# Kernel optimization log

Measured on AMD Instinct MI355X. Metric: run time of the kernel, lower is better.

Reference implementation:

```python
import jax, jax.numpy as jnp
import numpy as np

N, W, T = 8, 64, 8192      # batch, emb_width, time
K_BINS = 2048

def setup_inputs() -> dict:
    key = jax.random.key(0)
    kx, kk = jax.random.split(key)
    x = jax.random.normal(kx, (N, W, T), dtype=jnp.float32)
    k = jax.random.normal(kk, (K_BINS, W), dtype=jnp.float32)
    return {"x": x, "k": k}

def reference(x, k):
    n, w, t = x.shape
    # preprocess: (N, W, T) -> (N*T, W)
    xf = jnp.transpose(x, (0, 2, 1)).reshape(-1, w)
    prenorm = jnp.linalg.norm(xf - jnp.mean(xf)) / np.sqrt(float(xf.size))
    # quantise: squared-euclidean distances via matmul expansion
    # dist[i, j] = ||xf_i||^2 - 2 xf_i . k_j + ||k_j||^2   -> (N*T, K_BINS)
    dist = (jnp.sum(xf * xf, axis=-1, keepdims=True)
            - 2.0 * (xf @ k.T)
            + jnp.sum(k * k, axis=-1)[None, :])
    x_l = jnp.argmin(dist, axis=-1)            # (N*T,)
    fit = jnp.mean(jnp.min(dist, axis=-1))
    # dequantise: embedding gather
    x_d = k[x_l]                               # (N*T, W)
    commit_loss = jnp.sum((jax.lax.stop_gradient(x_d) - xf) ** 2) / float(xf.size)
    # straight-through estimator
    x_d = xf + jax.lax.stop_gradient(x_d - xf)
    # postprocess
    x_l = x_l.reshape(n, t)
    x_d = jnp.transpose(x_d.reshape(n, t, w), (0, 2, 1))  # (N, W, T)
    return x_l, x_d, commit_loss, fit, prenorm
```

## Files before the change

kernel.cpp:

```cpp
#include <hip/hip_runtime.h>
#include <hip/hip_bf16.h>
#include <math.h>

#define N_BATCH 8
#define WDIM 64
#define TDIM 8192
#define KBINS 2048
#define NROWS (N_BATCH * TDIM)
#define XSIZE (N_BATCH * WDIM * TDIM)
#define XL_OFF 0
#define XD_OFF NROWS
#define SCAL_OFF (NROWS + XSIZE)

#define MT 64
#define XST 72
#define TAU 0.05f
#define MAXFLAG 8192
#define NBLK (NROWS / MT)

#define WS_K2_OFF   0
#define WS_CNT_OFF  8192
#define WS_FLAG_OFF 8256
#define WS_SLOT_OFF 41024
#define WS_PART_OFF 106560
#define WS_KF_OFF   122944

typedef __attribute__((ext_vector_type(8))) short bf16x8;
typedef __attribute__((ext_vector_type(4))) float f32x4;
typedef unsigned long long u64;

static __device__ __forceinline__ short f2bf(float v) {
  __hip_bfloat16 b = __float2bfloat16(v);
  return *reinterpret_cast<short*>(&b);
}
static __device__ __forceinline__ float bf2f(short s) {
  unsigned int u = ((unsigned int)(unsigned short)s) << 16;
  return __uint_as_float(u);
}

#define GLOAD_LDS(gsrc, ldst)                                            \
  __builtin_amdgcn_global_load_lds(                                      \
      (const __attribute__((address_space(1))) unsigned int*)(gsrc),     \
      (__attribute__((address_space(3))) unsigned int*)(ldst), 16, 0, 0)

#define WAIT_VM4 0x0F74
#define WAIT_VM0 0x0F70

__global__ void prep_kernel(const float* __restrict__ kg, float* __restrict__ k2,
                            char* __restrict__ kfrag,
                            int* __restrict__ cnt, u64* __restrict__ slots) {
  __shared__ float skc[16 * 65];
  const int tid  = threadIdx.x;
  const int tile = blockIdx.x;
  const int c0   = tile * 16;
  if (tile == 0 && tid == 0) *cnt = 0;
  if (tid < 64) slots[tile * 64 + tid] = ~0ULL;
  {
    const float4* g4 = (const float4*)(kg + (size_t)c0 * WDIM);
    int code = tid >> 4, w = (tid & 15) * 4;
    *(float4*)&skc[code * 65 + w] = g4[tid];
  }
  __syncthreads();
  if (tid < 16) {
    const float* kr = &skc[tid * 65];
    float r[8];
#pragma unroll
    for (int l = 0; l < 8; ++l) r[l] = __fmul_rn(kr[l], kr[l]);
    for (int i = 8; i < WDIM; i += 8) {
#pragma unroll
      for (int l = 0; l < 8; ++l)
        r[l] = __fadd_rn(r[l], __fmul_rn(kr[i + l], kr[i + l]));
    }
    k2[c0 + tid] = __fadd_rn(__fadd_rn(__fadd_rn(r[0], r[1]), __fadd_rn(r[2], r[3])),
                             __fadd_rn(__fadd_rn(r[4], r[5]), __fadd_rn(r[6], r[7])));
  }
  {
    const int sub  = tid >> 6;
    const int lane = tid & 63;
    const int lcol = lane & 15;
    const int quad = lane >> 4;
    const float* src = &skc[lcol * 65 + (sub & 1) * 32 + quad * 8];
    const bool lo = (sub >= 2);
    short tmp[8];
#pragma unroll
    for (int i = 0; i < 8; ++i) {
      float v = src[i];
      short h = f2bf(v);
      tmp[i] = lo ? f2bf(v - bf2f(h)) : h;
    }
    char* dst = kfrag + (size_t)tile * 4096 + sub * 1024 + lane * 16;
    *(bf16x8*)dst = *(const bf16x8*)tmp;
  }
}

__launch_bounds__(128, 2)
__global__ void vq_mfma(const float* __restrict__ x,
                        const float* __restrict__ kg,
                        const float* __restrict__ k2g,
                        const char* __restrict__ kfrag,
                        float* __restrict__ out,
                        float* __restrict__ part,
                        int* __restrict__ flag_cnt,
                        int* __restrict__ flags) {
  __shared__ __align__(16) char smem[33408];
  char*  kbuf  = smem;
  float* k2f   = (float*)(smem + 24576);
  int*   sIdx      = (int*)  (smem + 32768);
  float* sPair     = (float*)(smem + 33024);
  int*   sFlagCnt  = (int*)  (smem + 33088);
  int*   sFlagBase = (int*)  (smem + 33092);
  int*   sFlagList = (int*)  (smem + 33096);
  short* sxh = (short*)smem;
  short* sxl = (short*)(smem + 9216);
  float* kd  = (float*)smem;

  const int tid  = threadIdx.x;
  const int blk  = blockIdx.x;
  const int row0 = blk * MT;
  const int n    = row0 >> 13;
  const int t0   = row0 & (TDIM - 1);

  if (tid == 0) *sFlagCnt = 0;

  const int r  = tid & 63;
  const int wh = tid >> 6;
  float x2p = 0.f, sxp = 0.f;
  const float* xb = x + (size_t)n * WDIM * TDIM + t0 + r;
#pragma unroll 8
  for (int i = 0; i < 32; ++i) {
    int w = 2 * i + wh;
    float v = xb[(size_t)w * TDIM];
    x2p = fmaf(v, v, x2p);
    sxp += v;
    short h = f2bf(v);
    sxh[r * XST + w] = h;
    sxl[r * XST + w] = f2bf(v - bf2f(h));
  }
  {
    const float4* k24 = (const float4*)k2g;
#pragma unroll
    for (int i = 0; i < 4; ++i) {
      int j = tid + i * 128;
      *(float4*)&k2f[j * 4] = k24[j];
    }
  }
  __syncthreads();

  const int wave = tid >> 6;
  const int lane = tid & 63;
  const int lcol = lane & 15;
  const int quad = lane >> 4;
  const int rA0 = wave * 32 + lcol;
  const int rA1 = wave * 32 + 16 + lcol;
  bf16x8 a0h0 = *(const bf16x8*)&sxh[rA0 * XST + 0  + quad * 8];
  bf16x8 a0h1 = *(const bf16x8*)&sxh[rA0 * XST + 32 + quad * 8];
  bf16x8 a0l0 = *(const bf16x8*)&sxl[rA0 * XST + 0  + quad * 8];
  bf16x8 a0l1 = *(const bf16x8*)&sxl[rA0 * XST + 32 + quad * 8];
  bf16x8 a1h0 = *(const bf16x8*)&sxh[rA1 * XST + 0  + quad * 8];
  bf16x8 a1h1 = *(const bf16x8*)&sxh[rA1 * XST + 32 + quad * 8];
  bf16x8 a1l0 = *(const bf16x8*)&sxl[rA1 * XST + 0  + quad * 8];
  bf16x8 a1l1 = *(const bf16x8*)&sxl[rA1 * XST + 32 + quad * 8];
  __syncthreads();

  float bd[8], b2[8];
  int   bi[8];
#pragma unroll
  for (int i = 0; i < 8; ++i) { bd[i] = 3.0e38f; b2[i] = 3.0e38f; bi[i] = 0; }

  char* mybuf = kbuf + wave * 12288;
  const char* kfg = kfrag;

#define VQ_ISSUE(C, B)                                                       \
  if ((C) < 128) {                                                           \
    const char* s = kfg + (size_t)(C) * 4096 + (lane << 4);                  \
    char* d = mybuf + (B) * 4096;                                            \
    GLOAD_LDS(s, d);                                                         \
    GLOAD_LDS(s + 1024, d + 1024);                                           \
    GLOAD_LDS(s + 2048, d + 2048);                                           \
    GLOAD_LDS(s + 3072, d + 3072);                                           \
  }

#define VQ_STEP(C, RB, PB, WAITIMM)                                          \
  {                                                                          \
    __builtin_amdgcn_s_waitcnt(WAITIMM);                                     \
    const char* tb = mybuf + (RB) * 4096;                                    \
    bf16x8 bh0 = *(const bf16x8*)(tb + 0    + (lane << 4));                  \
    bf16x8 bh1 = *(const bf16x8*)(tb + 1024 + (lane << 4));                  \
    bf16x8 bl0 = *(const bf16x8*)(tb + 2048 + (lane << 4));                  \
    bf16x8 bl1 = *(const bf16x8*)(tb + 3072 + (lane << 4));                  \
    float k2c = k2f[(C) * 16 + lcol];                                        \
    VQ_ISSUE((C) + 2, PB)                                                    \
    f32x4 p0 = {0.f, 0.f, 0.f, 0.f};                                         \
    f32x4 p1 = {0.f, 0.f, 0.f, 0.f};                                         \
    p0 = __builtin_amdgcn_mfma_f32_16x16x32_bf16(a0h0, bh0, p0, 0, 0, 0);    \
    p1 = __builtin_amdgcn_mfma_f32_16x16x32_bf16(a1h0, bh0, p1, 0, 0, 0);    \
    p0 = __builtin_amdgcn_mfma_f32_16x16x32_bf16(a0h1, bh1, p0, 0, 0, 0);    \
    p1 = __builtin_amdgcn_mfma_f32_16x16x32_bf16(a1h1, bh1, p1, 0, 0, 0);    \
    p0 = __builtin_amdgcn_mfma_f32_16x16x32_bf16(a0h0, bl0, p0, 0, 0, 0);    \
    p1 = __builtin_amdgcn_mfma_f32_16x16x32_bf16(a1h0, bl0, p1, 0, 0, 0);    \
    p0 = __builtin_amdgcn_mfma_f32_16x16x32_bf16(a0h1, bl1, p0, 0, 0, 0);    \
    p1 = __builtin_amdgcn_mfma_f32_16x16x32_bf16(a1h1, bl1, p1, 0, 0, 0);    \
    p0 = __builtin_amdgcn_mfma_f32_16x16x32_bf16(a0l0, bh0, p0, 0, 0, 0);    \
    p1 = __builtin_amdgcn_mfma_f32_16x16x32_bf16(a1l0, bh0, p1, 0, 0, 0);    \
    p0 = __builtin_amdgcn_mfma_f32_16x16x32_bf16(a0l1, bh1, p0, 0, 0, 0);    \
    p1 = __builtin_amdgcn_mfma_f32_16x16x32_bf16(a1l1, bh1, p1, 0, 0, 0);    \
    const int code = (C) * 16 + lcol;                                        \
    _Pragma("unroll")                                                        \
    for (int i = 0; i < 4; ++i) {                                            \
      float d0 = fmaf(-2.f, p0[i], k2c);                                     \
      float nb2a = __builtin_amdgcn_fmed3f(bd[i], d0, b2[i]);                \
      bool lt0 = d0 < bd[i];                                                 \
      bd[i] = lt0 ? d0 : bd[i];                                              \
      bi[i] = lt0 ? code : bi[i];                                            \
      b2[i] = nb2a;                                                          \
      float d1 = fmaf(-2.f, p1[i], k2c);                                     \
      float nb2b = __builtin_amdgcn_fmed3f(bd[4 + i], d1, b2[4 + i]);        \
      bool lt1 = d1 < bd[4 + i];                                             \
      bd[4 + i] = lt1 ? d1 : bd[4 + i];                                      \
      bi[4 + i] = lt1 ? code : bi[4 + i];                                    \
      b2[4 + i] = nb2b;                                                      \
    }                                                                        \
  }

  VQ_ISSUE(0, 0)
  VQ_ISSUE(1, 1)
  for (int c = 0; c < 126; c += 3) {
    VQ_STEP(c,     0, 2, WAIT_VM4)
    VQ_STEP(c + 1, 1, 0, WAIT_VM4)
    VQ_STEP(c + 2, 2, 1, WAIT_VM4)
  }
  VQ_STEP(126, 0, 2, WAIT_VM4)
  VQ_STEP(127, 1, 0, WAIT_VM0)
#undef VQ_STEP
#undef VQ_ISSUE

#pragma unroll
  for (int m = 1; m < 16; m <<= 1) {
#pragma unroll
    for (int i = 0; i < 8; ++i) {
      float od  = __shfl_xor(bd[i], m, 64);
      float od2 = __shfl_xor(b2[i], m, 64);
      int   oi  = __shfl_xor(bi[i], m, 64);
      float nb2 = fminf(fminf(b2[i], od2), fmaxf(bd[i], od));
      bool take = (od < bd[i]) || (od == bd[i] && oi < bi[i]);
      bd[i] = take ? od : bd[i];
      bi[i] = take ? oi : bi[i];
      b2[i] = nb2;
    }
  }

  float fit_p = 0.f;
  if (lcol == 0) {
#pragma unroll
    for (int i = 0; i < 8; ++i) {
      int s = i >> 2, ii = i & 3;
      int rloc = wave * 32 + s * 16 + quad * 4 + ii;
      int rowg = row0 + rloc;
      out[XL_OFF + rowg] = (float)bi[i];
      sIdx[rloc] = bi[i];
      fit_p += bd[i];
      if (b2[i] - bd[i] < TAU) {
        int slot = atomicAdd(sFlagCnt, 1);
        sFlagList[slot] = rowg;
      }
    }
  }
  __syncthreads();

  int nloc = *sFlagCnt;
  if (tid == 0 && nloc > 0) *sFlagBase = atomicAdd(flag_cnt, nloc);
  __syncthreads();
  if (tid < nloc) {
    int gs = *sFlagBase + tid;
    if (gs < MAXFLAG) flags[gs] = sFlagList[tid];
  }

  {
    int rr = tid >> 1, half = tid & 1;
    const float4* kr4 = (const float4*)(kg + (size_t)sIdx[rr] * WDIM + half * 32);
    float4* dst = (float4*)&kd[rr * 68 + half * 32];
#pragma unroll
    for (int j = 0; j < 8; ++j) dst[j] = kr4[j];
  }
  __syncthreads();

  float commit_p = 0.f;
  float* xdb = out + XD_OFF + (size_t)n * WDIM * TDIM + t0 + r;
#pragma unroll 8
  for (int i = 0; i < 32; ++i) {
    int w = 2 * i + wh;
    float xvv = xb[(size_t)w * TDIM];
    float kvv = kd[r * 68 + w];
    float df = kvv - xvv;
    commit_p = fmaf(df, df, commit_p);
    xdb[(size_t)w * TDIM] = kvv;
  }

  float v0 = sxp, v1 = x2p, v2 = commit_p, v3 = fit_p;
#pragma unroll
  for (int off = 32; off > 0; off >>= 1) {
    v0 += __shfl_down(v0, off, 64);
    v1 += __shfl_down(v1, off, 64);
    v2 += __shfl_down(v2, off, 64);
    v3 += __shfl_down(v3, off, 64);
  }
  if (lane == 0) {
    sPair[wave * 4 + 0] = v0;
    sPair[wave * 4 + 1] = v1;
    sPair[wave * 4 + 2] = v2;
    sPair[wave * 4 + 3] = v3;
  }
  __syncthreads();
  if (tid == 0) {
    float x2sum = sPair[1] + sPair[5];
    part[0 * NBLK + blk] = sPair[0] + sPair[4];
    part[1 * NBLK + blk] = x2sum;
    part[2 * NBLK + blk] = sPair[2] + sPair[6];
    part[3 * NBLK + blk] = (sPair[3] + sPair[7]) + x2sum;
  }
}

__launch_bounds__(256, 4)
__global__ void recheck_scan(const float* __restrict__ x,
                             const float* __restrict__ kg,
                             const float* __restrict__ k2g,
                             const int* __restrict__ flag_cnt,
                             const int* __restrict__ flags,
                             u64* __restrict__ slots) {
  __shared__ float sx[WDIM];
  __shared__ float sx2s;
  const int tid = threadIdx.x;
  int nf = *flag_cnt;
  if (nf > MAXFLAG) nf = MAXFLAG;
  const int total = nf * 8;

  for (int g = blockIdx.x; g < total; g += 2048) {
    const int fi  = g >> 3;
    const int seg = g & 7;
    const int row = flags[fi];
    const int n = row >> 13;
    const int t = row & (TDIM - 1);
    if (tid < WDIM) sx[tid] = x[(size_t)n * WDIM * TDIM + (size_t)tid * TDIM + t];
    __syncthreads();
    if (tid == 0) {
      float r8[8];
#pragma unroll
      for (int l = 0; l < 8; ++l) r8[l] = __fmul_rn(sx[l], sx[l]);
      for (int i = 8; i < WDIM; i += 8) {
#pragma unroll
        for (int l = 0; l < 8; ++l)
          r8[l] = __fadd_rn(r8[l], __fmul_rn(sx[i + l], sx[i + l]));
      }
      sx2s = __fadd_rn(__fadd_rn(__fadd_rn(r8[0], r8[1]), __fadd_rn(r8[2], r8[3])),
                       __fadd_rn(__fadd_rn(r8[4], r8[5]), __fadd_rn(r8[6], r8[7])));
    }
    __syncthreads();

    const int j = seg * 256 + tid;
    const float* kr = kg + (size_t)j * WDIM;
    float c = 0.f;
#pragma unroll
    for (int w = 0; w < WDIM; ++w)
      c = __fmaf_rn(sx[w], kr[w], c);
    float d = __fadd_rn(__fsub_rn(sx2s, __fmul_rn(2.0f, c)), k2g[j]);

    u64 key = ((u64)__float_as_uint(d) << 32) | (unsigned int)j;
#pragma unroll
    for (int off = 32; off > 0; off >>= 1) {
      u64 o = __shfl_down((unsigned long long)key, off, 64);
      if (o < key) key = o;
    }
    if ((tid & 63) == 0) atomicMin(&slots[fi], key);
    __syncthreads();
  }
}

__global__ void recheck_write(const float* __restrict__ kg,
                              const int* __restrict__ flag_cnt,
                              const int* __restrict__ flags,
                              const u64* __restrict__ slots,
                              float* __restrict__ out) {
  int nf = *flag_cnt;
  if (nf > MAXFLAG) nf = MAXFLAG;
  const int w = threadIdx.x;
  for (int fi = blockIdx.x; fi < nf; fi += 256) {
    const int row = flags[fi];
    const int n = row >> 13;
    const int t = row & (TDIM - 1);
    const int j = (int)(slots[fi] & 0xFFFFFFFFULL);
    if (w == 0) out[XL_OFF + row] = (float)j;
    out[XD_OFF + (size_t)n * WDIM * TDIM + (size_t)w * TDIM + t] = kg[(size_t)j * WDIM + w];
  }
}

__global__ void finalize_kernel(const float* __restrict__ part, float* __restrict__ out) {
  __shared__ double sred[4][64];
  const int tid = threadIdx.x;
  const int lane = tid & 63;
  const int wv = tid >> 6;
  double a[4] = {0.0, 0.0, 0.0, 0.0};
  for (int i = tid; i < NBLK; i += 256) {
#pragma unroll
    for (int q = 0; q < 4; ++q) a[q] += (double)part[q * NBLK + i];
  }
#pragma unroll
  for (int off = 32; off > 0; off >>= 1) {
#pragma unroll
    for (int q = 0; q < 4; ++q)
      a[q] += __shfl_down(a[q], off, 64);
  }
  if (lane == 0) {
#pragma unroll
    for (int q = 0; q < 4; ++q) sred[q][wv] = a[q];
  }
  __syncthreads();
  if (tid == 0) {
    double s0 = 0, s1 = 0, s2 = 0, s3 = 0;
#pragma unroll
    for (int wv2 = 0; wv2 < 4; ++wv2) {
      s0 += sred[0][wv2]; s1 += sred[1][wv2];
      s2 += sred[2][wv2]; s3 += sred[3][wv2];
    }
    double size = (double)XSIZE;
    double commit = s2 / size;
    double fit = s3 / (double)NROWS;
    double mean = s0 / size;
    double var = s1 / size - mean * mean;
    if (var < 0.0) var = 0.0;
    out[SCAL_OFF + 0] = (float)commit;
    out[SCAL_OFF + 1] = (float)fit;
    out[SCAL_OFF + 2] = (float)sqrt(var);
  }
}

extern "C" void kernel_launch(void* const* d_in, const int* in_sizes, int n_in,
                              void* d_out, int out_size, void* d_ws, size_t ws_size,
                              hipStream_t stream) {
  const float* x = (const float*)d_in[0];
  const float* kg = (const float*)d_in[1];
  float* out = (float*)d_out;
  float* k2   = (float*)((char*)d_ws + WS_K2_OFF);
  int* cnt    = (int*)((char*)d_ws + WS_CNT_OFF);
  int* flags  = (int*)((char*)d_ws + WS_FLAG_OFF);
  u64* slots  = (u64*)((char*)d_ws + WS_SLOT_OFF);
  float* part = (float*)((char*)d_ws + WS_PART_OFF);
  char* kfrag = (char*)d_ws + WS_KF_OFF;

  hipLaunchKernelGGL(prep_kernel, dim3(KBINS / 16), dim3(256), 0, stream,
                     kg, k2, kfrag, cnt, slots);
  hipLaunchKernelGGL(vq_mfma, dim3(NBLK), dim3(128), 0, stream,
                     x, kg, k2, kfrag, out, part, cnt, flags);
  hipLaunchKernelGGL(recheck_scan, dim3(2048), dim3(256), 0, stream,
                     x, kg, k2, cnt, flags, slots);
  hipLaunchKernelGGL(recheck_write, dim3(256), dim3(WDIM), 0, stream,
                     kg, cnt, flags, slots, out);
  hipLaunchKernelGGL(finalize_kernel, dim3(1), dim3(256), 0, stream, part, out);
}
```

Baseline: 201.9 us.

## Share codebook LDS buffers across four waves and add transposed codebook for recheck

The main kernel moves from 2 waves each owning 32 rows with private triple-buffered codebook tiles to 4 waves of 16 rows each. The waves share one triple buffer filled by wave 0 and synchronised with a barrier every step. This cuts LDS per block and raises occupancy, but adds a block-wide barrier per codebook chunk and halves the MFMA reuse of each B fragment per wave. Separately, the prep kernel writes a transposed copy of the codebook so the recheck scan can read it coalesced when the workspace is large enough.

Measured after the change: 167.3 us. 1.21x faster.

```diff
diff --git a/kernel.cpp b/kernel.cpp
--- a/kernel.cpp
+++ b/kernel.cpp
@@ -24,6 +24,8 @@
 #define WS_SLOT_OFF 41024
 #define WS_PART_OFF 106560
 #define WS_KF_OFF   122944
+#define WS_KT_OFF   647296
+#define WS_KT_END   (WS_KT_OFF + (size_t)WDIM * KBINS * 4)
 
 typedef __attribute__((ext_vector_type(8))) short bf16x8;
 typedef __attribute__((ext_vector_type(4))) float f32x4;
@@ -46,8 +48,10 @@
 #define WAIT_VM4 0x0F74
 #define WAIT_VM0 0x0F70
 
+#define SBAR() asm volatile("s_barrier" ::: "memory")
+
 __global__ void prep_kernel(const float* __restrict__ kg, float* __restrict__ k2,
-                            char* __restrict__ kfrag,
+                            char* __restrict__ kfrag, float* __restrict__ kT,
                             int* __restrict__ cnt, u64* __restrict__ slots) {
   __shared__ float skc[16 * 65];
   const int tid  = threadIdx.x;
@@ -74,6 +78,14 @@
     k2[c0 + tid] = __fadd_rn(__fadd_rn(__fadd_rn(r[0], r[1]), __fadd_rn(r[2], r[3])),
                              __fadd_rn(__fadd_rn(r[4], r[5]), __fadd_rn(r[6], r[7])));
   }
+  if (kT) {
+    const int code = tid & 15;
+#pragma unroll
+    for (int j = 0; j < 4; ++j) {
+      int w = (tid >> 4) + 16 * j;
+      kT[(size_t)w * KBINS + c0 + code] = skc[code * 65 + w];
+    }
+  }
   {
     const int sub  = tid >> 6;
     const int lane = tid & 63;
@@ -93,7 +105,7 @@
   }
 }
 
-__launch_bounds__(128, 2)
+__launch_bounds__(256, 4)
 __global__ void vq_mfma(const float* __restrict__ x,
                         const float* __restrict__ kg,
                         const float* __restrict__ k2g,
@@ -102,17 +114,17 @@
                         float* __restrict__ part,
                         int* __restrict__ flag_cnt,
                         int* __restrict__ flags) {
-  __shared__ __align__(16) char smem[33408];
-  char*  kbuf  = smem;
-  float* k2f   = (float*)(smem + 24576);
-  int*   sIdx      = (int*)  (smem + 32768);
-  float* sPair     = (float*)(smem + 33024);
-  int*   sFlagCnt  = (int*)  (smem + 33088);
-  int*   sFlagBase = (int*)  (smem + 33092);
-  int*   sFlagList = (int*)  (smem + 33096);
+  __shared__ __align__(16) char smem[20480];
+  char*  kbuf = smem;
+  float* k2f  = (float*)(smem + 12288);
   short* sxh = (short*)smem;
   short* sxl = (short*)(smem + 9216);
   float* kd  = (float*)smem;
+  int*   sIdx      = (int*)  (smem + 18432);
+  float* sPair     = (float*)(smem + 18688);
+  int*   sFlagCnt  = (int*)  (smem + 18752);
+  int*   sFlagBase = (int*)  (smem + 18756);
+  int*   sFlagList = (int*)  (smem + 18760);
 
   const int tid  = threadIdx.x;
   const int blk  = blockIdx.x;
@@ -120,15 +132,13 @@
   const int n    = row0 >> 13;
   const int t0   = row0 & (TDIM - 1);
 
-  if (tid == 0) *sFlagCnt = 0;
-
   const int r  = tid & 63;
   const int wh = tid >> 6;
   float x2p = 0.f, sxp = 0.f;
   const float* xb = x + (size_t)n * WDIM * TDIM + t0 + r;
 #pragma unroll 8
-  for (int i = 0; i < 32; ++i) {
-    int w = 2 * i + wh;
+  for (int i = 0; i < 16; ++i) {
+    int w = 4 * i + wh;
     float v = xb[(size_t)w * TDIM];
     x2p = fmaf(v, v, x2p);
     sxp += v;
@@ -136,94 +146,77 @@
     sxh[r * XST + w] = h;
     sxl[r * XST + w] = f2bf(v - bf2f(h));
   }
-  {
-    const float4* k24 = (const float4*)k2g;
-#pragma unroll
-    for (int i = 0; i < 4; ++i) {
-      int j = tid + i * 128;
-      *(float4*)&k2f[j * 4] = k24[j];
-    }
-  }
   __syncthreads();
 
   const int wave = tid >> 6;
   const int lane = tid & 63;
   const int lcol = lane & 15;
   const int quad = lane >> 4;
-  const int rA0 = wave * 32 + lcol;
-  const int rA1 = wave * 32 + 16 + lcol;
-  bf16x8 a0h0 = *(const bf16x8*)&sxh[rA0 * XST + 0  + quad * 8];
-  bf16x8 a0h1 = *(const bf16x8*)&sxh[rA0 * XST + 32 + quad * 8];
-  bf16x8 a0l0 = *(const bf16x8*)&sxl[rA0 * XST + 0  + quad * 8];
-  bf16x8 a0l1 = *(const bf16x8*)&sxl[rA0 * XST + 32 + quad * 8];
-  bf16x8 a1h0 = *(const bf16x8*)&sxh[rA1 * XST + 0  + quad * 8];
-  bf16x8 a1h1 = *(const bf16x8*)&sxh[rA1 * XST + 32 + quad * 8];
-  bf16x8 a1l0 = *(const bf16x8*)&sxl[rA1 * XST + 0  + quad * 8];
-  bf16x8 a1l1 = *(const bf16x8*)&sxl[rA1 * XST + 32 + quad * 8];
-  __syncthreads();
-
-  float bd[8], b2[8];
-  int   bi[8];
-#pragma unroll
-  for (int i = 0; i < 8; ++i) { bd[i] = 3.0e38f; b2[i] = 3.0e38f; bi[i] = 0; }
-
-  char* mybuf = kbuf + wave * 12288;
+  const int rA = wave * 16 + lcol;
+  bf16x8 ah0 = *(const bf16x8*)&sxh[rA * XST + 0  + quad * 8];
+  bf16x8 ah1 = *(const bf16x8*)&sxh[rA * XST + 32 + quad * 8];
+  bf16x8 al0 = *(const bf16x8*)&sxl[rA * XST + 0  + quad * 8];
+  bf16x8 al1 = *(const bf16x8*)&sxl[rA * XST + 32 + quad * 8];
+  __syncthreads();
+
+  float bd[4], b2[4];
+  int   bi[4];
+#pragma unroll
+  for (int i = 0; i < 4; ++i) { bd[i] = 3.0e38f; b2[i] = 3.0e38f; bi[i] = 0; }
+
   const char* kfg = kfrag;
 
 #define VQ_ISSUE(C, B)                                                       \
   if ((C) < 128) {                                                           \
     const char* s = kfg + (size_t)(C) * 4096 + (lane << 4);                  \
-    char* d = mybuf + (B) * 4096;                                            \
+    char* d = kbuf + (B) * 4096;                                             \
     GLOAD_LDS(s, d);                                                         \
     GLOAD_LDS(s + 1024, d + 1024);                                           \
     GLOAD_LDS(s + 2048, d + 2048);                                           \
     GLOAD_LDS(s + 3072, d + 3072);                                           \
   }
 
+  if (wave == 0) {
+    VQ_ISSUE(0, 0)
+    VQ_ISSUE(1, 1)
+  }
+  {
+    const float4* k24 = (const float4*)k2g;
+    *(float4*)&k2f[tid * 8]     = k24[tid * 2];
+    *(float4*)&k2f[tid * 8 + 4] = k24[tid * 2 + 1];
+  }
+  asm volatile("s_waitcnt lgkmcnt(0)\n\ts_barrier" ::: "memory");
+
 #define VQ_STEP(C, RB, PB, WAITIMM)                                          \
   {                                                                          \
-    __builtin_amdgcn_s_waitcnt(WAITIMM);                                     \
-    const char* tb = mybuf + (RB) * 4096;                                    \
+    if (wave == 0) __builtin_amdgcn_s_waitcnt(WAITIMM);                      \
+    SBAR();                                                                  \
+    const char* tb = kbuf + (RB) * 4096;                                     \
     bf16x8 bh0 = *(const bf16x8*)(tb + 0    + (lane << 4));                  \
     bf16x8 bh1 = *(const bf16x8*)(tb + 1024 + (lane << 4));                  \
     bf16x8 bl0 = *(const bf16x8*)(tb + 2048 + (lane << 4));                  \
     bf16x8 bl1 = *(const bf16x8*)(tb + 3072 + (lane << 4));                  \
     float k2c = k2f[(C) * 16 + lcol];                                        \
-    VQ_ISSUE((C) + 2, PB)                                                    \
-    f32x4 p0 = {0.f, 0.f, 0.f, 0.f};                                         \
-    f32x4 p1 = {0.f, 0.f, 0.f, 0.f};                                         \
-    p0 = __builtin_amdgcn_mfma_f32_16x16x32_bf16(a0h0, bh0, p0, 0, 0, 0);    \
-    p1 = __builtin_amdgcn_mfma_f32_16x16x32_bf16(a1h0, bh0, p1, 0, 0, 0);    \
-    p0 = __builtin_amdgcn_mfma_f32_16x16x32_bf16(a0h1, bh1, p0, 0, 0, 0);    \
-    p1 = __builtin_amdgcn_mfma_f32_16x16x32_bf16(a1h1, bh1, p1, 0, 0, 0);    \
-    p0 = __builtin_amdgcn_mfma_f32_16x16x32_bf16(a0h0, bl0, p0, 0, 0, 0);    \
-    p1 = __builtin_amdgcn_mfma_f32_16x16x32_bf16(a1h0, bl0, p1, 0, 0, 0);    \
-    p0 = __builtin_amdgcn_mfma_f32_16x16x32_bf16(a0h1, bl1, p0, 0, 0, 0);    \
-    p1 = __builtin_amdgcn_mfma_f32_16x16x32_bf16(a1h1, bl1, p1, 0, 0, 0);    \
-    p0 = __builtin_amdgcn_mfma_f32_16x16x32_bf16(a0l0, bh0, p0, 0, 0, 0);    \
-    p1 = __builtin_amdgcn_mfma_f32_16x16x32_bf16(a1l0, bh0, p1, 0, 0, 0);    \
-    p0 = __builtin_amdgcn_mfma_f32_16x16x32_bf16(a0l1, bh1, p0, 0, 0, 0);    \
-    p1 = __builtin_amdgcn_mfma_f32_16x16x32_bf16(a1l1, bh1, p1, 0, 0, 0);    \
+    if (wave == 0) { VQ_ISSUE((C) + 2, PB) }                                 \
+    f32x4 p = {0.f, 0.f, 0.f, 0.f};                                          \
+    p = __builtin_amdgcn_mfma_f32_16x16x32_bf16(ah0, bh0, p, 0, 0, 0);       \
+    p = __builtin_amdgcn_mfma_f32_16x16x32_bf16(ah1, bh1, p, 0, 0, 0);       \
+    p = __builtin_amdgcn_mfma_f32_16x16x32_bf16(ah0, bl0, p, 0, 0, 0);       \
+    p = __builtin_amdgcn_mfma_f32_16x16x32_bf16(ah1, bl1, p, 0, 0, 0);       \
+    p = __builtin_amdgcn_mfma_f32_16x16x32_bf16(al0, bh0, p, 0, 0, 0);       \
+    p = __builtin_amdgcn_mfma_f32_16x16x32_bf16(al1, bh1, p, 0, 0, 0);       \
     const int code = (C) * 16 + lcol;                                        \
     _Pragma("unroll")                                                        \
     for (int i = 0; i < 4; ++i) {                                            \
-      float d0 = fmaf(-2.f, p0[i], k2c);                                     \
-      float nb2a = __builtin_amdgcn_fmed3f(bd[i], d0, b2[i]);                \
+      float d0 = fmaf(-2.f, p[i], k2c);                                      \
+      float nb2 = __builtin_amdgcn_fmed3f(bd[i], d0, b2[i]);                 \
       bool lt0 = d0 < bd[i];                                                 \
       bd[i] = lt0 ? d0 : bd[i];                                              \
       bi[i] = lt0 ? code : bi[i];                                            \
-      b2[i] = nb2a;                                                          \
-      float d1 = fmaf(-2.f, p1[i], k2c);                                     \
-      float nb2b = __builtin_amdgcn_fmed3f(bd[4 + i], d1, b2[4 + i]);        \
-      bool lt1 = d1 < bd[4 + i];                                             \
-      bd[4 + i] = lt1 ? d1 : bd[4 + i];                                      \
-      bi[4 + i] = lt1 ? code : bi[4 + i];                                    \
-      b2[4 + i] = nb2b;                                                      \
+      b2[i] = nb2;                                                           \
     }                                                                        \
   }
 
-  VQ_ISSUE(0, 0)
-  VQ_ISSUE(1, 1)
   for (int c = 0; c < 126; c += 3) {
     VQ_STEP(c,     0, 2, WAIT_VM4)
     VQ_STEP(c + 1, 1, 0, WAIT_VM4)
@@ -237,7 +230,7 @@
 #pragma unroll
   for (int m = 1; m < 16; m <<= 1) {
 #pragma unroll
-    for (int i = 0; i < 8; ++i) {
+    for (int i = 0; i < 4; ++i) {
       float od  = __shfl_xor(bd[i], m, 64);
       float od2 = __shfl_xor(b2[i], m, 64);
       int   oi  = __shfl_xor(bi[i], m, 64);
@@ -249,12 +242,15 @@
     }
   }
 
+  __syncthreads();
+  if (tid == 0) *sFlagCnt = 0;
+  __syncthreads();
+
   float fit_p = 0.f;
   if (lcol == 0) {
 #pragma unroll
-    for (int i = 0; i < 8; ++i) {
-      int s = i >> 2, ii = i & 3;
-      int rloc = wave * 32 + s * 16 + quad * 4 + ii;
+    for (int i = 0; i < 4; ++i) {
+      int rloc = wave * 16 + quad * 4 + i;
       int rowg = row0 + rloc;
       out[XL_OFF + rowg] = (float)bi[i];
       sIdx[rloc] = bi[i];
@@ -276,19 +272,19 @@
   }
 
   {
-    int rr = tid >> 1, half = tid & 1;
-    const float4* kr4 = (const float4*)(kg + (size_t)sIdx[rr] * WDIM + half * 32);
-    float4* dst = (float4*)&kd[rr * 68 + half * 32];
-#pragma unroll
-    for (int j = 0; j < 8; ++j) dst[j] = kr4[j];
+    int rr = tid >> 2, q4 = tid & 3;
+    const float4* kr4 = (const float4*)(kg + (size_t)sIdx[rr] * WDIM) + q4 * 4;
+    float4* dst = (float4*)&kd[rr * 68 + q4 * 16];
+#pragma unroll
+    for (int j = 0; j < 4; ++j) dst[j] = kr4[j];
   }
   __syncthreads();
 
   float commit_p = 0.f;
   float* xdb = out + XD_OFF + (size_t)n * WDIM * TDIM + t0 + r;
 #pragma unroll 8
-  for (int i = 0; i < 32; ++i) {
-    int w = 2 * i + wh;
+  for (int i = 0; i < 16; ++i) {
+    int w = 4 * i + wh;
     float xvv = xb[(size_t)w * TDIM];
     float kvv = kd[r * 68 + w];
     float df = kvv - xvv;
@@ -312,17 +308,18 @@
   }
   __syncthreads();
   if (tid == 0) {
-    float x2sum = sPair[1] + sPair[5];
-    part[0 * NBLK + blk] = sPair[0] + sPair[4];
+    float x2sum = sPair[1] + sPair[5] + sPair[9] + sPair[13];
+    part[0 * NBLK + blk] = sPair[0] + sPair[4] + sPair[8] + sPair[12];
     part[1 * NBLK + blk] = x2sum;
-    part[2 * NBLK + blk] = sPair[2] + sPair[6];
-    part[3 * NBLK + blk] = (sPair[3] + sPair[7]) + x2sum;
+    part[2 * NBLK + blk] = sPair[2] + sPair[6] + sPair[10] + sPair[14];
+    part[3 * NBLK + blk] = (sPair[3] + sPair[7] + sPair[11] + sPair[15]) + x2sum;
   }
 }
 
 __launch_bounds__(256, 4)
 __global__ void recheck_scan(const float* __restrict__ x,
                              const float* __restrict__ kg,
+                             const float* __restrict__ kT,
                              const float* __restrict__ k2g,
                              const int* __restrict__ flag_cnt,
                              const int* __restrict__ flags,
@@ -357,11 +354,17 @@
     __syncthreads();
 
     const int j = seg * 256 + tid;
-    const float* kr = kg + (size_t)j * WDIM;
     float c = 0.f;
-#pragma unroll
-    for (int w = 0; w < WDIM; ++w)
-      c = __fmaf_rn(sx[w], kr[w], c);
+    if (kT) {
+#pragma unroll
+      for (int w = 0; w < WDIM; ++w)
+        c = __fmaf_rn(sx[w], kT[(size_t)w * KBINS + j], c);
+    } else {
+      const float* kr = kg + (size_t)j * WDIM;
+#pragma unroll
+      for (int w = 0; w < WDIM; ++w)
+        c = __fmaf_rn(sx[w], kr[w], c);
+    }
     float d = __fadd_rn(__fsub_rn(sx2s, __fmul_rn(2.0f, c)), k2g[j]);
 
     u64 key = ((u64)__float_as_uint(d) << 32) | (unsigned int)j;
@@ -445,13 +448,14 @@
   u64* slots  = (u64*)((char*)d_ws + WS_SLOT_OFF);
   float* part = (float*)((char*)d_ws + WS_PART_OFF);
   char* kfrag = (char*)d_ws + WS_KF_OFF;
+  float* kT   = (ws_size >= WS_KT_END) ? (float*)((char*)d_ws + WS_KT_OFF) : nullptr;
 
   hipLaunchKernelGGL(prep_kernel, dim3(KBINS / 16), dim3(256), 0, stream,
-                     kg, k2, kfrag, cnt, slots);
-  hipLaunchKernelGGL(vq_mfma, dim3(NBLK), dim3(128), 0, stream,
+                     kg, k2, kfrag, kT, cnt, slots);
+  hipLaunchKernelGGL(vq_mfma, dim3(NBLK), dim3(256), 0, stream,
                      x, kg, k2, kfrag, out, part, cnt, flags);
   hipLaunchKernelGGL(recheck_scan, dim3(2048), dim3(256), 0, stream,
-                     x, kg, k2, cnt, flags, slots);
+                     x, kg, kT, k2, cnt, flags, slots);
   hipLaunchKernelGGL(recheck_write, dim3(256), dim3(WDIM), 0, stream,
                      kg, cnt, flags, slots, out);
   hipLaunchKernelGGL(finalize_kernel, dim3(1), dim3(256), 0, stream, part, out);
```
